# Optimization experiments

Hardware: AMD Instinct MI355X
Metric: run time of the kernel (lower is better)

## Reference

```python
import jax, jax.numpy as jnp
import numpy as np

B, S, HID = 2, 2048, 2560
NH, NKV, HD = 8, 4, 256
Q_SIZE, KV_SIZE = NH * HD, NKV * HD
SCALE = 256.0 ** -0.5
SLIDING_WINDOW = 1024 - 1  # config.sliding_window - 1
ROPE_BASE = 10000.0
EPS = 1e-6


def rmsnorm(x, w, eps=EPS):
    xf = x.astype(jnp.float32)
    out = xf * jax.lax.rsqrt(jnp.mean(xf * xf, axis=-1, keepdims=True) + eps)
    return (out * (1.0 + w.astype(jnp.float32))).astype(x.dtype)


def apply_rope(x, positions):
    # x: [B,S,H,D], neox style (rotate halves)
    d = x.shape[-1]
    inv_freq = 1.0 / (ROPE_BASE ** (jnp.arange(0, d, 2, dtype=jnp.float32) / d))
    freqs = positions.astype(jnp.float32)[..., None] * inv_freq  # [B,S,d/2]
    cos = jnp.cos(freqs)[:, :, None, :]
    sin = jnp.sin(freqs)[:, :, None, :]
    x1, x2 = x[..., : d // 2], x[..., d // 2:]
    return jnp.concatenate([x1 * cos - x2 * sin, x2 * cos + x1 * sin], axis=-1).astype(x.dtype)


def setup_inputs() -> dict:
    key = jax.random.key(0)
    ks = jax.random.split(key, 4)
    positions = jnp.broadcast_to(jnp.arange(S, dtype=jnp.int32)[None, :], (B, S))
    hidden_states = jax.random.normal(ks[0], (B, S, HID), dtype=jnp.float32)
    attention_mask = jnp.ones((B, S), dtype=jnp.int32)
    Wqkv = jax.random.normal(ks[1], (HID, Q_SIZE + 2 * KV_SIZE), dtype=jnp.float32) * (HID ** -0.5)
    Wo = jax.random.normal(ks[2], (Q_SIZE, HID), dtype=jnp.float32) * (Q_SIZE ** -0.5)
    q_norm_w = jnp.zeros((HD,), dtype=jnp.float32)
    k_norm_w = jnp.zeros((HD,), dtype=jnp.float32)
    return {"positions": positions, "hidden_states": hidden_states,
            "attention_mask": attention_mask, "Wqkv": Wqkv, "Wo": Wo,
            "q_norm_w": q_norm_w, "k_norm_w": k_norm_w}


def reference(positions, hidden_states, attention_mask, Wqkv, Wo, q_norm_w, k_norm_w):
    b, s, _ = hidden_states.shape
    qkv = hidden_states @ Wqkv
    q, k, v = jnp.split(qkv, [Q_SIZE, Q_SIZE + KV_SIZE], axis=-1)
    q = q.reshape(b, s, NH, HD)
    k = k.reshape(b, s, NKV, HD)
    v = v.reshape(b, s, NKV, HD)
    q = rmsnorm(q, q_norm_w)
    k = rmsnorm(k, k_norm_w)
    q = apply_rope(q, positions)
    k = apply_rope(k, positions)

    # additive mask, replicating source exactly
    idx = jnp.arange(s)
    causal = idx[None, :] > idx[:, None]             # triu(diag=1)
    too_far = (idx[None, :] - idx[:, None]) > SLIDING_WINDOW
    base_mask = causal | too_far                      # [S,S]
    key_pad = attention_mask.astype(bool) == False    # [B,S]
    masked = base_mask[None, None, :, :] | key_pad[:, None, None, :]  # [B,1,S,S]
    add_mask = jnp.where(masked, -jnp.inf, 0.0).astype(jnp.float32)

    # GQA: group queries over kv heads
    g = NH // NKV
    qg = q.reshape(b, s, NKV, g, HD)
    scores = jnp.einsum('bsmgd,btmd->bmgst', qg, k) * SCALE  # [B,NKV,g,S,S]
    scores = scores + add_mask[:, :, None, :, :]
    probs = jax.nn.softmax(scores, axis=-1)
    out = jnp.einsum('bmgst,btmd->bsmgd', probs, v)           # [B,S,NKV,g,HD]
    out = out.reshape(b, s, NH * HD)
    return out @ Wo
```

## Files before the change

kernel.cpp:

```cpp
#include <hip/hip_runtime.h>
#include <stdint.h>

#define S_LEN 2048
#define BATCH 2
#define HIDDEN 2560
#define NH 8
#define NKV 4
#define HD 256
#define QSZ (NH*HD)
#define NQKV 4096
#define MROWS (BATCH*S_LEN)
#define SCALE_ATT 0.0625f

using bf16x8 = __attribute__((__ext_vector_type__(8))) __bf16;
using f32x4  = __attribute__((__ext_vector_type__(4))) float;
using s16x8  = __attribute__((__ext_vector_type__(8))) short;

union B8u { s16x8 s; bf16x8 b; };
union I4B8 { int4 i; bf16x8 b; };

__device__ __forceinline__ unsigned short f2bf(float x){
  unsigned u = __float_as_uint(x);
  u += 0x7fffu + ((u >> 16) & 1u);
  return (unsigned short)(u >> 16);
}
__device__ __forceinline__ float bf2f(unsigned short h){
  return __uint_as_float(((unsigned)h) << 16);
}
__device__ __forceinline__ bf16x8 ld_bf8(const unsigned short* p){
  B8u u; u.s = *reinterpret_cast<const s16x8*>(p); return u.b;
}
__device__ __forceinline__ f32x4 mfma16(bf16x8 a, bf16x8 b, f32x4 c){
  return __builtin_amdgcn_mfma_f32_16x16x32_bf16(a, b, c, 0, 0, 0);
}
__device__ __forceinline__ void gload16(const void* g, void* l){
  __builtin_amdgcn_global_load_lds((const __attribute__((address_space(1))) void*)g,
                                   (__attribute__((address_space(3))) void*)l,
                                   16, 0, 0);
}
__device__ __forceinline__ int cvtpk(float lo, float hi){
  int r;
  asm("v_cvt_pk_bf16_f32 %0, %1, %2" : "=v"(r) : "v"(lo), "v"(hi));
  return r;
}

__global__ __launch_bounds__(256) void cast_bf16_kernel(
    const float* __restrict__ in, unsigned short* __restrict__ out, int n)
{
  int i = (blockIdx.x * 256 + threadIdx.x) * 4;
  if (i < n){
    float4 v = *reinterpret_cast<const float4*>(in + i);
    ushort4 o;
    o.x = f2bf(v.x); o.y = f2bf(v.y); o.z = f2bf(v.z); o.w = f2bf(v.w);
    *reinterpret_cast<ushort4*>(out + i) = o;
  }
}

__global__ __launch_bounds__(256) void tcast_kernel(
    const float* __restrict__ in, unsigned short* __restrict__ out, int R, int C)
{
  __shared__ float t[32][33];
  int c0 = blockIdx.x * 32, r0 = blockIdx.y * 32;
  int tx = threadIdx.x & 31, ty = threadIdx.x >> 5;
#pragma unroll
  for (int ii = 0; ii < 4; ii++)
    t[ty + ii*8][tx] = in[(size_t)(r0 + ty + ii*8) * C + c0 + tx];
  __syncthreads();
#pragma unroll
  for (int ii = 0; ii < 4; ii++)
    out[(size_t)(c0 + ty + ii*8) * R + r0 + tx] = f2bf(t[tx][ty + ii*8]);
}

template<int BF16OUT>
__global__ __launch_bounds__(512, 2) void gemm256_kernel(
    const unsigned short* __restrict__ A,
    const unsigned short* __restrict__ BT,
    void* __restrict__ Cv,
    int N, int K, int nbn)
{
  __shared__ unsigned short Ab[2][256 * 64];
  __shared__ unsigned short Bb[2][256 * 64];

  const int tid  = threadIdx.x;
  const int lane = tid & 63;
  const int wid  = tid >> 6;
  const int wm = wid >> 2, wn = wid & 3;
  const int lq = lane & 15, lk = lane >> 4;

  const int cpx = gridDim.x >> 3;
  const int wg  = (blockIdx.x & 7) * cpx + (blockIdx.x >> 3);
  const int bm = wg / nbn, bn = wg % nbn;

  const int l8 = lane >> 3;
  const int sl = ((lane & 7) ^ l8) * 8;
  const unsigned short* agS = A  + (size_t)(bm*256 + wid*16 + l8) * K + sl;
  const unsigned short* bgS = BT + (size_t)(bn*256 + wid*16 + l8) * K + sl;

  f32x4 acc[4][4][2] = {};
  bf16x8 a[4][2], b[2][2];

#define STA(c, h, tt) do {                                                    \
    unsigned short* d = &Ab[c][(h)*8192 + wid*1024];                          \
    const unsigned short* s = agS + (size_t)(h)*128*K + (size_t)(tt)*64;      \
    gload16(s, d); gload16(s + 8*(size_t)K, d + 512);                         \
  } while (0)
#define STB(c, h, tt) do {                                                    \
    unsigned short* d = &Bb[c][(h)*8192 + wid*1024];                          \
    const unsigned short* s = bgS + (size_t)(h)*128*K + (size_t)(tt)*64;      \
    gload16(s, d); gload16(s + 8*(size_t)K, d + 512);                         \
  } while (0)
#define LDA(qa) do {                                                          \
    _Pragma("unroll") for (int m = 0; m < 4; m++)                             \
    _Pragma("unroll") for (int kk = 0; kk < 2; kk++)                          \
      a[m][kk] = ld_bf8(&Ab[cur][((qa)*128 + wm*64 + m*16 + lq)*64            \
                                 + (((kk*4 + lk) ^ (lq & 7)) << 3)]);         \
  } while (0)
#define LDB(qb) do {                                                          \
    _Pragma("unroll") for (int n = 0; n < 2; n++)                             \
    _Pragma("unroll") for (int kk = 0; kk < 2; kk++)                          \
      b[n][kk] = ld_bf8(&Bb[cur][((qb)*128 + wn*32 + n*16 + lq)*64            \
                                 + (((kk*4 + lk) ^ (lq & 7)) << 3)]);         \
  } while (0)
#define MM(qi) do {                                                           \
    __builtin_amdgcn_s_setprio(1);                                            \
    _Pragma("unroll") for (int m = 0; m < 4; m++)                             \
    _Pragma("unroll") for (int n = 0; n < 2; n++)                             \
    _Pragma("unroll") for (int kk = 0; kk < 2; kk++)                          \
      acc[qi][m][n] = mfma16(a[m][kk], b[n][kk], acc[qi][m][n]);              \
    __builtin_amdgcn_s_setprio(0);                                            \
  } while (0)
#define BARR __builtin_amdgcn_s_barrier()
#define VM(n) asm volatile("s_waitcnt vmcnt(" #n ")" ::: "memory")

  STA(0, 0, 0); STB(0, 0, 0); STB(0, 1, 0); STA(0, 1, 0);
  VM(4); BARR;

  const int NT = K >> 6;
  for (int t = 0; t < NT - 1; ++t){
    const int cur = t & 1, nxt = cur ^ 1;
    LDA(0); LDB(0); STA(nxt, 0, t+1);
    BARR; MM(0); VM(4); BARR;
    LDB(1);         STB(nxt, 0, t+1);
    BARR; MM(1); VM(4); BARR;
    LDA(1);         STB(nxt, 1, t+1);
    BARR; MM(2);        BARR;
    LDB(0);         STA(nxt, 1, t+1);
    BARR; MM(3); VM(4); BARR;
  }
  {
    const int cur = (NT - 1) & 1;
    LDA(0); LDB(0); BARR; MM(0); VM(2); BARR;
    LDB(1);         BARR; MM(1); VM(0); BARR;
    LDA(1);         BARR; MM(2);        BARR;
    LDB(0);         BARR; MM(3);        BARR;
  }
#undef STA
#undef STB
#undef LDA
#undef LDB
#undef MM
#undef BARR
#undef VM

#pragma unroll
  for (int qi = 0; qi < 4; qi++){
    const int qa = qi >> 1;
    const int qb = (qi ^ (qi >> 1)) & 1;
    const int r0 = bm*256 + qa*128 + wm*64;
    const int c0 = bn*256 + qb*128 + wn*32;
#pragma unroll
    for (int m = 0; m < 4; m++)
#pragma unroll
      for (int n = 0; n < 2; n++)
#pragma unroll
        for (int i = 0; i < 4; i++){
          const size_t idx = (size_t)(r0 + m*16 + lk*4 + i) * N + (c0 + n*16 + lq);
          if (BF16OUT) ((unsigned short*)Cv)[idx] = f2bf(acc[qi][m][n][i]);
          else         ((float*)Cv)[idx]          = acc[qi][m][n][i];
        }
  }
}

__global__ __launch_bounds__(256) void normrope_kernel(
    const unsigned short* __restrict__ qkv,
    const int* __restrict__ positions,
    const float* __restrict__ qw, const float* __restrict__ kw,
    unsigned short* __restrict__ qB,
    unsigned short* __restrict__ kB,
    unsigned short* __restrict__ vT)
{
  const int s = blockIdx.x, b = blockIdx.y;
  const int lane = threadIdx.x & 63, wid = threadIdx.x >> 6;
  const unsigned short* row = qkv + (size_t)(b * S_LEN + s) * NQKV;
  const float fpos = (float)positions[b * S_LEN + s];

#pragma unroll
  for (int t = 0; t < 4; t++){
    const int seg = t * 4 + wid;
    const int base = seg * HD;
    float x0 = bf2f(row[base + lane]);
    float x1 = bf2f(row[base + lane + 64]);
    float x2 = bf2f(row[base + lane + 128]);
    float x3 = bf2f(row[base + lane + 192]);
    if (seg >= 12){
      const int mh = seg - 12;
      unsigned short* vb = vT + (size_t)(b * NKV + mh) * HD * S_LEN + s;
      vb[(size_t)(lane      ) * S_LEN] = f2bf(x0);
      vb[(size_t)(lane +  64) * S_LEN] = f2bf(x1);
      vb[(size_t)(lane + 128) * S_LEN] = f2bf(x2);
      vb[(size_t)(lane + 192) * S_LEN] = f2bf(x3);
    } else {
      const float* w = (seg < 8) ? qw : kw;
      float ssq = x0*x0 + x1*x1 + x2*x2 + x3*x3;
#pragma unroll
      for (int d = 1; d < 64; d <<= 1) ssq += __shfl_xor(ssq, d, 64);
      float rs = rsqrtf(ssq * (1.0f / 256.0f) + 1e-6f);
      float y0 = x0 * rs * (1.0f + w[lane]);
      float y1 = x1 * rs * (1.0f + w[lane + 64]);
      float y2 = x2 * rs * (1.0f + w[lane + 128]);
      float y3 = x3 * rs * (1.0f + w[lane + 192]);
      const float kln = -9.210340371976184f / 128.0f;
      float inv1 = expf((float)lane * kln);
      float inv2 = expf((float)(lane + 64) * kln);
      float s1, c1, s2, c2;
      sincosf(fpos * inv1, &s1, &c1);
      sincosf(fpos * inv2, &s2, &c2);
      float o0 = y0 * c1 - y2 * s1;
      float o2 = y2 * c1 + y0 * s1;
      float o1 = y1 * c2 - y3 * s2;
      float o3 = y3 * c2 + y1 * s2;
      unsigned short* dst = (seg < 8)
        ? qB + ((size_t)(b * NH  +  seg     ) * S_LEN + s) * HD
        : kB + ((size_t)(b * NKV + (seg - 8)) * S_LEN + s) * HD;
      dst[lane      ] = f2bf(o0);
      dst[lane +  64] = f2bf(o1);
      dst[lane + 128] = f2bf(o2);
      dst[lane + 192] = f2bf(o3);
    }
  }
}

__global__ void maskbits_kernel(const int* __restrict__ amask, unsigned* __restrict__ bm,
                                int* __restrict__ ctr)
{
  int t = threadIdx.x;
  int b = t >> 6, tile = t & 63;
  unsigned m = 0;
  for (int j = 0; j < 32; j++)
    m |= (amask[b * S_LEN + tile * 32 + j] != 0 ? 1u : 0u) << j;
  bm[t] = m;
  if (t < 8) ctr[t] = 0;
}

__global__ __launch_bounds__(256) void attn_kernel(
    const unsigned short* __restrict__ qB,
    const unsigned short* __restrict__ kB,
    const unsigned short* __restrict__ vT,
    const unsigned* __restrict__ bmG,
    unsigned short* __restrict__ attnO,
    int* __restrict__ ctr)
{
  __shared__ unsigned short Kb[2][32 * 256];
  __shared__ unsigned short Vb[2][256 * 32];
  __shared__ unsigned bm_lds[64];
  __shared__ int s_idx;

  const int tid  = threadIdx.x;
  const int lane = tid & 63, wid = tid >> 6;
  const int c  = blockIdx.x & 7;
  const int mh = c & 3, b = c >> 2;
  const int h  = mh * 2 + (wid >> 1);
  const int lq = lane & 15, lk = lane >> 4;

  if (tid < 64) bm_lds[tid] = bmG[(b << 6) + tid];

  const unsigned short* kbase = kB + (size_t)(b * NKV + mh) * S_LEN * HD;
  const unsigned short* vbase = vT + (size_t)(b * NKV + mh) * HD * S_LEN;
  const int krow0 = wid * 2 + (lane >> 5);
  const int kgsrc = (lane & 31) ^ (krow0 & 7);
  const unsigned short* kg0 = kbase + (size_t)krow0 * HD + kgsrc * 8;
  const int vd0 = wid * 16 + (lane >> 2);
  const int vgsrc = (lane & 3) ^ ((lane >> 3) & 3);
  const unsigned short* vg0 = vbase + (size_t)vd0 * S_LEN + vgsrc * 8;

#define STAGE_K(buf, ktv)                                                      \
  do {                                                                         \
    _Pragma("unroll")                                                          \
    for (int r = 0; r < 4; r++)                                                \
      gload16(kg0 + (size_t)(ktv) * HD + r * (8 * HD),                         \
              &Kb[buf][wid * 512 + r * 2048]);                                 \
  } while (0)
#define STAGE_V(buf, ktv)                                                      \
  do {                                                                         \
    _Pragma("unroll")                                                          \
    for (int r = 0; r < 4; r++)                                                \
      gload16(vg0 + (ktv) + (size_t)r * (64 * S_LEN),                          \
              &Vb[buf][wid * 512 + r * 2048]);                                 \
  } while (0)

  for (;;){
    if (tid == 0) s_idx = atomicAdd(&ctr[c], 1);
    __syncthreads();
    const int idx = s_idx;
    __syncthreads();
    if (idx >= 64) break;
    const int qt = 63 - idx;

    const int q0 = qt * 32 + (wid & 1) * 16;
    const int q  = q0 + lq;

    const unsigned short* qbase = qB + ((size_t)(b * NH + h) * S_LEN + q0 + lq) * HD + lk * 8;
    bf16x8 aq[8];
#pragma unroll
    for (int ks = 0; ks < 8; ks++) aq[ks] = ld_bf8(qbase + ks * 32);
    asm volatile("s_waitcnt vmcnt(0)" ::: "memory");

    float mi = -__builtin_inff(), li = 0.f;
    f32x4 oacc[16] = {};

    const int ktmax = qt * 32;

    STAGE_K(0, 0);  STAGE_V(0, 0);
    if (ktmax >= 32){ STAGE_K(1, 32); STAGE_V(1, 32); }

    int cur = 0;
    for (int kt = 0; kt <= ktmax; kt += 32, cur ^= 1){
      if (kt < ktmax) asm volatile("s_waitcnt vmcnt(8)" ::: "memory");
      else            asm volatile("s_waitcnt vmcnt(0)" ::: "memory");
      __syncthreads();

      f32x4 s0 = {0.f,0.f,0.f,0.f}, s1 = {0.f,0.f,0.f,0.f};
#pragma unroll
      for (int ks = 0; ks < 8; ks++){
        const int slot = (((ks * 4 + lk) ^ (lq & 7)) << 3);
        bf16x8 kf0 = ld_bf8(&Kb[cur][lq * 256 + slot]);
        bf16x8 kf1 = ld_bf8(&Kb[cur][(16 + lq) * 256 + slot]);
        s0 = mfma16(kf0, aq[ks], s0);
        s1 = mfma16(kf1, aq[ks], s1);
      }

      const unsigned mask32 = bm_lds[kt >> 5];
      const int koff = lk * 4;
      float v0[4], v1[4];
#pragma unroll
      for (int j2 = 0; j2 < 4; j2++){
        const bool cc0 = (kt + koff + j2 <= q)      && ((mask32 >> (koff + j2)) & 1u);
        const bool cc1 = (kt + 16 + koff + j2 <= q) && ((mask32 >> (16 + koff + j2)) & 1u);
        v0[j2] = cc0 ? s0[j2] * SCALE_ATT : -__builtin_inff();
        v1[j2] = cc1 ? s1[j2] * SCALE_ATT : -__builtin_inff();
      }
      float tm = fmaxf(fmaxf(fmaxf(v0[0], v0[1]), fmaxf(v0[2], v0[3])),
                       fmaxf(fmaxf(v1[0], v1[1]), fmaxf(v1[2], v1[3])));
      tm = fmaxf(tm, __shfl_xor(tm, 16, 64));
      tm = fmaxf(tm, __shfl_xor(tm, 32, 64));

      float p0[4], p1[4];
      if (__all(tm <= mi + 8.0f)){
        const float mns = fmaxf(mi, -1e30f);
#pragma unroll
        for (int j2 = 0; j2 < 4; j2++){
          p0[j2] = __expf(v0[j2] - mns);
          p1[j2] = __expf(v1[j2] - mns);
        }
        float rs = (p0[0] + p0[1]) + (p0[2] + p0[3]) + (p1[0] + p1[1]) + (p1[2] + p1[3]);
        rs += __shfl_xor(rs, 16, 64);
        rs += __shfl_xor(rs, 32, 64);
        li += rs;
      } else {
        const float mn  = fmaxf(mi, tm);
        const float mns = fmaxf(mn, -1e30f);
#pragma unroll
        for (int j2 = 0; j2 < 4; j2++){
          p0[j2] = __expf(v0[j2] - mns);
          p1[j2] = __expf(v1[j2] - mns);
        }
        const float a_ = __expf(mi - mns);
        float rs = (p0[0] + p0[1]) + (p0[2] + p0[3]) + (p1[0] + p1[1]) + (p1[2] + p1[3]);
        rs += __shfl_xor(rs, 16, 64);
        rs += __shfl_xor(rs, 32, 64);
        li = li * a_ + rs;
        mi = mn;
        float av[4];
#pragma unroll
        for (int i = 0; i < 4; i++)
          av[i] = __shfl(a_, (lane & 48) | (lk * 4 + i), 64);
#pragma unroll
        for (int db = 0; db < 16; db++){
          f32x4 o = oacc[db];
#pragma unroll
          for (int i = 0; i < 4; i++) o[i] *= av[i];
          oacc[db] = o;
        }
      }

      const int w0 = cvtpk(p0[0], p0[1]), w1 = cvtpk(p0[2], p0[3]);
      const int w2 = cvtpk(p1[0], p1[1]), w3 = cvtpk(p1[2], p1[3]);
      const int sA = (((lk & 1) * 2) << 4) | lq;
      const int sB = sA + 16;
      const int a0 = __shfl(w0, sA, 64), a1 = __shfl(w1, sA, 64);
      const int b0 = __shfl(w0, sB, 64), b1 = __shfl(w1, sB, 64);
      const int c0w = __shfl(w2, sA, 64), c1w = __shfl(w3, sA, 64);
      const int d0w = __shfl(w2, sB, 64), d1w = __shfl(w3, sB, 64);
      const bool hi = (lk >= 2);
      I4B8 pau;
      pau.i.x = hi ? c0w : a0;
      pau.i.y = hi ? c1w : a1;
      pau.i.z = hi ? d0w : b0;
      pau.i.w = hi ? d1w : b1;

      const int vslot = (lk ^ ((lq >> 1) & 3)) << 3;
#pragma unroll
      for (int db = 0; db < 16; db++){
        bf16x8 vf = ld_bf8(&Vb[cur][(db * 16 + lq) * 32 + vslot]);
        oacc[db] = mfma16(pau.b, vf, oacc[db]);
      }

      __syncthreads();
      if (kt + 64 <= ktmax){ STAGE_K(cur, kt + 64); STAGE_V(cur, kt + 64); }
    }

#pragma unroll
    for (int i = 0; i < 4; i++){
      const float lf = __shfl(li, (lane & 48) | (lk * 4 + i), 64);
      const float inv = 1.0f / lf;
      unsigned short* orow = attnO + (size_t)(b * S_LEN + q0 + lk*4 + i) * QSZ + h * HD + lq;
#pragma unroll
      for (int db = 0; db < 16; db++)
        orow[db * 16] = f2bf(oacc[db][i] * inv);
    }
  }
#undef STAGE_K
#undef STAGE_V
}

extern "C" void kernel_launch(void* const* d_in, const int* in_sizes, int n_in,
                              void* d_out, int out_size, void* d_ws, size_t ws_size,
                              hipStream_t stream)
{
  const int*   positions = (const int*)  d_in[0];
  const float* hidden    = (const float*)d_in[1];
  const int*   amask     = (const int*)  d_in[2];
  const float* Wqkv      = (const float*)d_in[3];
  const float* Wo        = (const float*)d_in[4];
  const float* qw        = (const float*)d_in[5];
  const float* kw        = (const float*)d_in[6];
  float* out = (float*)d_out;

  char* ws = (char*)d_ws;
  unsigned short* hB    = (unsigned short*)(ws);
  unsigned short* attnO = (unsigned short*)(ws);
  unsigned short* WqT   = (unsigned short*)(ws + 20971520);
  unsigned short* WoT   = (unsigned short*)(ws + 41943040);
  unsigned short* qkvB  = (unsigned short*)(ws + 52428800);
  unsigned short* qb    = (unsigned short*)(ws + 119537664);
  unsigned short* kb    = (unsigned short*)(ws + 136314880);
  unsigned short* vt    = (unsigned short*)(ws + 144703488);
  unsigned*       bm    = (unsigned*)     (ws + 153092096);
  int*            ctr   = (int*)          (ws + 153092608);

  cast_bf16_kernel<<<dim3(MROWS * HIDDEN / 1024), 256, 0, stream>>>(hidden, hB, MROWS * HIDDEN);
  tcast_kernel<<<dim3(NQKV / 32, HIDDEN / 32), 256, 0, stream>>>(Wqkv, WqT, HIDDEN, NQKV);
  tcast_kernel<<<dim3(HIDDEN / 32, QSZ / 32), 256, 0, stream>>>(Wo, WoT, QSZ, HIDDEN);
  maskbits_kernel<<<dim3(1), 128, 0, stream>>>(amask, bm, ctr);

  gemm256_kernel<1><<<dim3((MROWS/256) * (NQKV/256)), 512, 0, stream>>>(
      hB, WqT, qkvB, NQKV, HIDDEN, NQKV/256);

  normrope_kernel<<<dim3(S_LEN, BATCH), 256, 0, stream>>>(qkvB, positions, qw, kw, qb, kb, vt);

  attn_kernel<<<dim3(256), 256, 0, stream>>>(qb, kb, vt, bm, attnO, ctr);

  gemm256_kernel<0><<<dim3((MROWS/256) * (HIDDEN/256)), 512, 0, stream>>>(
      attnO, WoT, out, HIDDEN, QSZ, HIDDEN/256);
}
```

Before: 338.5 us.

## Split attention key range across wave pairs with LDS merge of partial softmax

Each work item now covers a 16-row query tile instead of 32, and the two waves per head split the key tiles into even and odd 32-key blocks, keeping separate online-softmax state. After the loop, one wave writes its partial output and max/sum to shared memory, and the other merges both with rescaling before writing bf16 output. K and V staging is split so K for the next step is prefetched during the softmax phase and V after the PV product. The grid doubles to 512 blocks to give finer-grained work units. The cost is extra barriers per iteration and an LDS merge pass at the end.

```diff
diff --git a/kernel.cpp b/kernel.cpp
--- a/kernel.cpp
+++ b/kernel.cpp
@@ -260,16 +260,18 @@
     unsigned short* __restrict__ attnO,
     int* __restrict__ ctr)
 {
-  __shared__ unsigned short Kb[2][32 * 256];
-  __shared__ unsigned short Vb[2][256 * 32];
+  __shared__ unsigned short Ks[2][32 * 256];
+  __shared__ unsigned short Vs[2][256 * 32];
   __shared__ unsigned bm_lds[64];
+  __shared__ float mlbuf[2][2][16];
   __shared__ int s_idx;
 
   const int tid  = threadIdx.x;
   const int lane = tid & 63, wid = tid >> 6;
   const int c  = blockIdx.x & 7;
   const int mh = c & 3, b = c >> 2;
-  const int h  = mh * 2 + (wid >> 1);
+  const int hh = wid >> 1, sp = wid & 1;
+  const int h  = mh * 2 + hh;
   const int lq = lane & 15, lk = lane >> 4;
 
   if (tid < 64) bm_lds[tid] = bmG[(b << 6) + tid];
@@ -283,19 +285,33 @@
   const int vgsrc = (lane & 3) ^ ((lane >> 3) & 3);
   const unsigned short* vg0 = vbase + (size_t)vd0 * S_LEN + vgsrc * 8;
 
-#define STAGE_K(buf, ktv)                                                      \
+  float* obuf = (float*)&Ks[0][0];
+
+#define STAGE_K2(it1)                                                          \
   do {                                                                         \
+    const int ka = min((it1) * 64,      S_LEN - 32);                           \
+    const int kb2 = min((it1) * 64 + 32, S_LEN - 32);                          \
     _Pragma("unroll")                                                          \
     for (int r = 0; r < 4; r++)                                                \
-      gload16(kg0 + (size_t)(ktv) * HD + r * (8 * HD),                         \
-              &Kb[buf][wid * 512 + r * 2048]);                                 \
-  } while (0)
-#define STAGE_V(buf, ktv)                                                      \
-  do {                                                                         \
+      gload16(kg0 + (size_t)ka * HD + r * (8 * HD),                            \
+              &Ks[0][wid * 512 + r * 2048]);                                   \
     _Pragma("unroll")                                                          \
     for (int r = 0; r < 4; r++)                                                \
-      gload16(vg0 + (ktv) + (size_t)r * (64 * S_LEN),                          \
-              &Vb[buf][wid * 512 + r * 2048]);                                 \
+      gload16(kg0 + (size_t)kb2 * HD + r * (8 * HD),                           \
+              &Ks[1][wid * 512 + r * 2048]);                                   \
+  } while (0)
+#define STAGE_V2(it1)                                                          \
+  do {                                                                         \
+    const int ka = min((it1) * 64,      S_LEN - 32);                           \
+    const int kb2 = min((it1) * 64 + 32, S_LEN - 32);                          \
+    _Pragma("unroll")                                                          \
+    for (int r = 0; r < 4; r++)                                                \
+      gload16(vg0 + ka  + (size_t)r * (64 * S_LEN),                            \
+              &Vs[0][wid * 512 + r * 2048]);                                   \
+    _Pragma("unroll")                                                          \
+    for (int r = 0; r < 4; r++)                                                \
+      gload16(vg0 + kb2 + (size_t)r * (64 * S_LEN),                            \
+              &Vs[1][wid * 512 + r * 2048]);                                   \
   } while (0)
 
   for (;;){
@@ -303,11 +319,12 @@
     __syncthreads();
     const int idx = s_idx;
     __syncthreads();
-    if (idx >= 64) break;
-    const int qt = 63 - idx;
-
-    const int q0 = qt * 32 + (wid & 1) * 16;
+    if (idx >= 128) break;
+    const int qt16 = 127 - idx;
+    const int q0 = qt16 * 16;
     const int q  = q0 + lq;
+    const int nt = (qt16 >> 1) + 1;
+    const int L  = (nt + 1) >> 1;
 
     const unsigned short* qbase = qB + ((size_t)(b * NH + h) * S_LEN + q0 + lq) * HD + lk * 8;
     bf16x8 aq[8];
@@ -318,28 +335,30 @@
     float mi = -__builtin_inff(), li = 0.f;
     f32x4 oacc[16] = {};
 
-    const int ktmax = qt * 32;
-
-    STAGE_K(0, 0);  STAGE_V(0, 0);
-    if (ktmax >= 32){ STAGE_K(1, 32); STAGE_V(1, 32); }
-
-    int cur = 0;
-    for (int kt = 0; kt <= ktmax; kt += 32, cur ^= 1){
-      if (kt < ktmax) asm volatile("s_waitcnt vmcnt(8)" ::: "memory");
-      else            asm volatile("s_waitcnt vmcnt(0)" ::: "memory");
+    STAGE_K2(0);
+    STAGE_V2(0);
+
+    for (int it = 0; it < L; ++it){
+      const bool more = (it + 1 < L);
+      const int kt = it * 64 + sp * 32;
+
+      asm volatile("s_waitcnt vmcnt(8)" ::: "memory");
       __syncthreads();
 
       f32x4 s0 = {0.f,0.f,0.f,0.f}, s1 = {0.f,0.f,0.f,0.f};
 #pragma unroll
       for (int ks = 0; ks < 8; ks++){
         const int slot = (((ks * 4 + lk) ^ (lq & 7)) << 3);
-        bf16x8 kf0 = ld_bf8(&Kb[cur][lq * 256 + slot]);
-        bf16x8 kf1 = ld_bf8(&Kb[cur][(16 + lq) * 256 + slot]);
+        bf16x8 kf0 = ld_bf8(&Ks[sp][lq * 256 + slot]);
+        bf16x8 kf1 = ld_bf8(&Ks[sp][(16 + lq) * 256 + slot]);
         s0 = mfma16(kf0, aq[ks], s0);
         s1 = mfma16(kf1, aq[ks], s1);
       }
 
-      const unsigned mask32 = bm_lds[kt >> 5];
+      __syncthreads();
+      if (more) STAGE_K2(it + 1);
+
+      const unsigned mask32 = bm_lds[(kt >> 5) & 63];
       const int koff = lk * 4;
       float v0[4], v1[4];
 #pragma unroll
@@ -408,29 +427,63 @@
       pau.i.z = hi ? d0w : b0;
       pau.i.w = hi ? d1w : b1;
 
+      if (more) asm volatile("s_waitcnt vmcnt(8)" ::: "memory");
+      else      asm volatile("s_waitcnt vmcnt(0)" ::: "memory");
+      __syncthreads();
+
       const int vslot = (lk ^ ((lq >> 1) & 3)) << 3;
 #pragma unroll
       for (int db = 0; db < 16; db++){
-        bf16x8 vf = ld_bf8(&Vb[cur][(db * 16 + lq) * 32 + vslot]);
+        bf16x8 vf = ld_bf8(&Vs[sp][(db * 16 + lq) * 32 + vslot]);
         oacc[db] = mfma16(pau.b, vf, oacc[db]);
       }
 
       __syncthreads();
-      if (kt + 64 <= ktmax){ STAGE_K(cur, kt + 64); STAGE_V(cur, kt + 64); }
+      if (more) STAGE_V2(it + 1);
     }
 
-#pragma unroll
-    for (int i = 0; i < 4; i++){
-      const float lf = __shfl(li, (lane & 48) | (lk * 4 + i), 64);
-      const float inv = 1.0f / lf;
-      unsigned short* orow = attnO + (size_t)(b * S_LEN + q0 + lk*4 + i) * QSZ + h * HD + lq;
+    if (sp){
+      if (lk == 0){
+        mlbuf[hh][0][lq] = mi;
+        mlbuf[hh][1][lq] = li;
+      }
 #pragma unroll
       for (int db = 0; db < 16; db++)
-        orow[db * 16] = f2bf(oacc[db][i] * inv);
+#pragma unroll
+        for (int i = 0; i < 4; i++)
+          obuf[hh * 4096 + (lk*4 + i) * 256 + db*16 + lq] = oacc[db][i];
     }
+    __syncthreads();
+    if (!sp){
+      const float m1 = mlbuf[hh][0][lq];
+      const float l1 = mlbuf[hh][1][lq];
+      const float ms  = fmaxf(mi, m1);
+      const float msf = fmaxf(ms, -1e30f);
+      const float a0f = __expf(mi - msf);
+      const float a1f = __expf(m1 - msf);
+      const float inv = 1.0f / (li * a0f + l1 * a1f);
+      const float s0f = a0f * inv, s1f = a1f * inv;
+      float sc0[4], sc1[4];
+#pragma unroll
+      for (int i = 0; i < 4; i++){
+        sc0[i] = __shfl(s0f, (lane & 48) | (lk*4 + i), 64);
+        sc1[i] = __shfl(s1f, (lane & 48) | (lk*4 + i), 64);
+      }
+#pragma unroll
+      for (int i = 0; i < 4; i++){
+        unsigned short* orow = attnO + (size_t)(b * S_LEN + q0 + lk*4 + i) * QSZ + h * HD + lq;
+#pragma unroll
+        for (int db = 0; db < 16; db++){
+          float v = oacc[db][i] * sc0[i]
+                  + obuf[hh * 4096 + (lk*4 + i) * 256 + db*16 + lq] * sc1[i];
+          orow[db * 16] = f2bf(v);
+        }
+      }
+    }
+    __syncthreads();
   }
-#undef STAGE_K
-#undef STAGE_V
+#undef STAGE_K2
+#undef STAGE_V2
 }
 
 extern "C" void kernel_launch(void* const* d_in, const int* in_sizes, int n_in,
@@ -468,7 +521,7 @@
 
   normrope_kernel<<<dim3(S_LEN, BATCH), 256, 0, stream>>>(qkvB, positions, qw, kw, qb, kb, vt);
 
-  attn_kernel<<<dim3(256), 256, 0, stream>>>(qb, kb, vt, bm, attnO, ctr);
+  attn_kernel<<<dim3(512), 256, 0, stream>>>(qb, kb, vt, bm, attnO, ctr);
 
   gemm256_kernel<0><<<dim3((MROWS/256) * (HIDDEN/256)), 512, 0, stream>>>(
       attnO, WoT, out, HIDDEN, QSZ, HIDDEN/256);
```

Measured after the change: 362.3 us. 7.0% more time.

## Process key tiles in pairs with four-deep K/V LDS pipeline

Applied to the files above, without the earlier changes.

The attention loop now handles two 32-key tiles per iteration, computing both score blocks before one shared online-softmax update, with one max/sum reduction and one rescale per pair. K/V staging grows from double to quadruple buffering, so more global loads are in flight and barriers per key tile are halved. The cost is double the LDS footprint (about 128KB), which may cut occupancy, plus extra registers for the second score block and branches for an odd final tile.

```diff
diff --git a/kernel.cpp b/kernel.cpp
--- a/kernel.cpp
+++ b/kernel.cpp
@@ -260,8 +260,8 @@
     unsigned short* __restrict__ attnO,
     int* __restrict__ ctr)
 {
-  __shared__ unsigned short Kb[2][32 * 256];
-  __shared__ unsigned short Vb[2][256 * 32];
+  __shared__ unsigned short Kb[4][32 * 256];
+  __shared__ unsigned short Vb[4][256 * 32];
   __shared__ unsigned bm_lds[64];
   __shared__ int s_idx;
 
@@ -318,51 +318,93 @@
     float mi = -__builtin_inff(), li = 0.f;
     f32x4 oacc[16] = {};
 
-    const int ktmax = qt * 32;
-
-    STAGE_K(0, 0);  STAGE_V(0, 0);
-    if (ktmax >= 32){ STAGE_K(1, 32); STAGE_V(1, 32); }
-
-    int cur = 0;
-    for (int kt = 0; kt <= ktmax; kt += 32, cur ^= 1){
-      if (kt < ktmax) asm volatile("s_waitcnt vmcnt(8)" ::: "memory");
-      else            asm volatile("s_waitcnt vmcnt(0)" ::: "memory");
+    STAGE_K(0, 0); STAGE_V(0, 0);
+    if (qt >= 1){ STAGE_K(1, 32); STAGE_V(1, 32); }
+    if (qt >= 2){ STAGE_K(2, 64); STAGE_V(2, 64); }
+    if (qt >= 3){ STAGE_K(3, 96); STAGE_V(3, 96); }
+
+    const int npairs = (qt >> 1) + 1;
+    for (int p = 0; p < npairs; ++p){
+      const int ktA = p * 64;
+      const int ktB = ktA + 32;
+      const bool hasB = (2*p + 1 <= qt);
+      const int bufA = (2*p) & 3, bufB = (2*p + 1) & 3;
+
+      const int ahead = qt - 2*p - 1;
+      if (ahead >= 2)      asm volatile("s_waitcnt vmcnt(16)" ::: "memory");
+      else if (ahead == 1) asm volatile("s_waitcnt vmcnt(8)"  ::: "memory");
+      else                 asm volatile("s_waitcnt vmcnt(0)"  ::: "memory");
       __syncthreads();
 
-      f32x4 s0 = {0.f,0.f,0.f,0.f}, s1 = {0.f,0.f,0.f,0.f};
-#pragma unroll
-      for (int ks = 0; ks < 8; ks++){
-        const int slot = (((ks * 4 + lk) ^ (lq & 7)) << 3);
-        bf16x8 kf0 = ld_bf8(&Kb[cur][lq * 256 + slot]);
-        bf16x8 kf1 = ld_bf8(&Kb[cur][(16 + lq) * 256 + slot]);
-        s0 = mfma16(kf0, aq[ks], s0);
-        s1 = mfma16(kf1, aq[ks], s1);
-      }
-
-      const unsigned mask32 = bm_lds[kt >> 5];
+      f32x4 sA0 = {0.f,0.f,0.f,0.f}, sA1 = {0.f,0.f,0.f,0.f};
+      f32x4 sB0 = {0.f,0.f,0.f,0.f}, sB1 = {0.f,0.f,0.f,0.f};
+      if (hasB){
+#pragma unroll
+        for (int ks = 0; ks < 8; ks++){
+          const int slot = (((ks * 4 + lk) ^ (lq & 7)) << 3);
+          bf16x8 kA0 = ld_bf8(&Kb[bufA][lq * 256 + slot]);
+          bf16x8 kA1 = ld_bf8(&Kb[bufA][(16 + lq) * 256 + slot]);
+          bf16x8 kB0 = ld_bf8(&Kb[bufB][lq * 256 + slot]);
+          bf16x8 kB1 = ld_bf8(&Kb[bufB][(16 + lq) * 256 + slot]);
+          sA0 = mfma16(kA0, aq[ks], sA0);
+          sA1 = mfma16(kA1, aq[ks], sA1);
+          sB0 = mfma16(kB0, aq[ks], sB0);
+          sB1 = mfma16(kB1, aq[ks], sB1);
+        }
+      } else {
+#pragma unroll
+        for (int ks = 0; ks < 8; ks++){
+          const int slot = (((ks * 4 + lk) ^ (lq & 7)) << 3);
+          bf16x8 kA0 = ld_bf8(&Kb[bufA][lq * 256 + slot]);
+          bf16x8 kA1 = ld_bf8(&Kb[bufA][(16 + lq) * 256 + slot]);
+          sA0 = mfma16(kA0, aq[ks], sA0);
+          sA1 = mfma16(kA1, aq[ks], sA1);
+        }
+      }
+
+      const unsigned mA = bm_lds[ktA >> 5];
+      const unsigned mB = bm_lds[(ktB >> 5) & 63];
       const int koff = lk * 4;
-      float v0[4], v1[4];
+      float vA0[4], vA1[4], vB0[4], vB1[4];
 #pragma unroll
       for (int j2 = 0; j2 < 4; j2++){
-        const bool cc0 = (kt + koff + j2 <= q)      && ((mask32 >> (koff + j2)) & 1u);
-        const bool cc1 = (kt + 16 + koff + j2 <= q) && ((mask32 >> (16 + koff + j2)) & 1u);
-        v0[j2] = cc0 ? s0[j2] * SCALE_ATT : -__builtin_inff();
-        v1[j2] = cc1 ? s1[j2] * SCALE_ATT : -__builtin_inff();
-      }
-      float tm = fmaxf(fmaxf(fmaxf(v0[0], v0[1]), fmaxf(v0[2], v0[3])),
-                       fmaxf(fmaxf(v1[0], v1[1]), fmaxf(v1[2], v1[3])));
+        const bool a0 = (ktA + koff + j2 <= q)      && ((mA >> (koff + j2)) & 1u);
+        const bool a1 = (ktA + 16 + koff + j2 <= q) && ((mA >> (16 + koff + j2)) & 1u);
+        vA0[j2] = a0 ? sA0[j2] * SCALE_ATT : -__builtin_inff();
+        vA1[j2] = a1 ? sA1[j2] * SCALE_ATT : -__builtin_inff();
+      }
+      if (hasB){
+#pragma unroll
+        for (int j2 = 0; j2 < 4; j2++){
+          const bool b0 = (ktB + koff + j2 <= q)      && ((mB >> (koff + j2)) & 1u);
+          const bool b1 = (ktB + 16 + koff + j2 <= q) && ((mB >> (16 + koff + j2)) & 1u);
+          vB0[j2] = b0 ? sB0[j2] * SCALE_ATT : -__builtin_inff();
+          vB1[j2] = b1 ? sB1[j2] * SCALE_ATT : -__builtin_inff();
+        }
+      } else {
+#pragma unroll
+        for (int j2 = 0; j2 < 4; j2++){ vB0[j2] = -__builtin_inff(); vB1[j2] = -__builtin_inff(); }
+      }
+      float tm = fmaxf(fmaxf(fmaxf(vA0[0], vA0[1]), fmaxf(vA0[2], vA0[3])),
+                       fmaxf(fmaxf(vA1[0], vA1[1]), fmaxf(vA1[2], vA1[3])));
+      if (hasB){
+        float tb = fmaxf(fmaxf(fmaxf(vB0[0], vB0[1]), fmaxf(vB0[2], vB0[3])),
+                         fmaxf(fmaxf(vB1[0], vB1[1]), fmaxf(vB1[2], vB1[3])));
+        tm = fmaxf(tm, tb);
+      }
       tm = fmaxf(tm, __shfl_xor(tm, 16, 64));
       tm = fmaxf(tm, __shfl_xor(tm, 32, 64));
 
-      float p0[4], p1[4];
+      float pA0[4], pA1[4], pB0[4], pB1[4];
       if (__all(tm <= mi + 8.0f)){
         const float mns = fmaxf(mi, -1e30f);
 #pragma unroll
         for (int j2 = 0; j2 < 4; j2++){
-          p0[j2] = __expf(v0[j2] - mns);
-          p1[j2] = __expf(v1[j2] - mns);
-        }
-        float rs = (p0[0] + p0[1]) + (p0[2] + p0[3]) + (p1[0] + p1[1]) + (p1[2] + p1[3]);
+          pA0[j2] = __expf(vA0[j2] - mns); pA1[j2] = __expf(vA1[j2] - mns);
+          pB0[j2] = __expf(vB0[j2] - mns); pB1[j2] = __expf(vB1[j2] - mns);
+        }
+        float rs = (pA0[0]+pA0[1])+(pA0[2]+pA0[3])+(pA1[0]+pA1[1])+(pA1[2]+pA1[3])
+                 + (pB0[0]+pB0[1])+(pB0[2]+pB0[3])+(pB1[0]+pB1[1])+(pB1[2]+pB1[3]);
         rs += __shfl_xor(rs, 16, 64);
         rs += __shfl_xor(rs, 32, 64);
         li += rs;
@@ -371,11 +413,12 @@
         const float mns = fmaxf(mn, -1e30f);
 #pragma unroll
         for (int j2 = 0; j2 < 4; j2++){
-          p0[j2] = __expf(v0[j2] - mns);
-          p1[j2] = __expf(v1[j2] - mns);
+          pA0[j2] = __expf(vA0[j2] - mns); pA1[j2] = __expf(vA1[j2] - mns);
+          pB0[j2] = __expf(vB0[j2] - mns); pB1[j2] = __expf(vB1[j2] - mns);
         }
         const float a_ = __expf(mi - mns);
-        float rs = (p0[0] + p0[1]) + (p0[2] + p0[3]) + (p1[0] + p1[1]) + (p1[2] + p1[3]);
+        float rs = (pA0[0]+pA0[1])+(pA0[2]+pA0[3])+(pA1[0]+pA1[1])+(pA1[2]+pA1[3])
+                 + (pB0[0]+pB0[1])+(pB0[2]+pB0[3])+(pB1[0]+pB1[1])+(pB1[2]+pB1[3]);
         rs += __shfl_xor(rs, 16, 64);
         rs += __shfl_xor(rs, 32, 64);
         li = li * a_ + rs;
@@ -393,30 +436,55 @@
         }
       }
 
-      const int w0 = cvtpk(p0[0], p0[1]), w1 = cvtpk(p0[2], p0[3]);
-      const int w2 = cvtpk(p1[0], p1[1]), w3 = cvtpk(p1[2], p1[3]);
-      const int sA = (((lk & 1) * 2) << 4) | lq;
-      const int sB = sA + 16;
-      const int a0 = __shfl(w0, sA, 64), a1 = __shfl(w1, sA, 64);
-      const int b0 = __shfl(w0, sB, 64), b1 = __shfl(w1, sB, 64);
-      const int c0w = __shfl(w2, sA, 64), c1w = __shfl(w3, sA, 64);
-      const int d0w = __shfl(w2, sB, 64), d1w = __shfl(w3, sB, 64);
+      const int sA_ = (((lk & 1) * 2) << 4) | lq;
+      const int sB_ = sA_ + 16;
       const bool hi = (lk >= 2);
-      I4B8 pau;
-      pau.i.x = hi ? c0w : a0;
-      pau.i.y = hi ? c1w : a1;
-      pau.i.z = hi ? d0w : b0;
-      pau.i.w = hi ? d1w : b1;
+      I4B8 pauA, pauB;
+      {
+        const int w0 = cvtpk(pA0[0], pA0[1]), w1 = cvtpk(pA0[2], pA0[3]);
+        const int w2 = cvtpk(pA1[0], pA1[1]), w3 = cvtpk(pA1[2], pA1[3]);
+        const int a0 = __shfl(w0, sA_, 64), a1 = __shfl(w1, sA_, 64);
+        const int b0 = __shfl(w0, sB_, 64), b1 = __shfl(w1, sB_, 64);
+        const int c0w = __shfl(w2, sA_, 64), c1w = __shfl(w3, sA_, 64);
+        const int d0w = __shfl(w2, sB_, 64), d1w = __shfl(w3, sB_, 64);
+        pauA.i.x = hi ? c0w : a0;
+        pauA.i.y = hi ? c1w : a1;
+        pauA.i.z = hi ? d0w : b0;
+        pauA.i.w = hi ? d1w : b1;
+      }
+      if (hasB){
+        const int w0 = cvtpk(pB0[0], pB0[1]), w1 = cvtpk(pB0[2], pB0[3]);
+        const int w2 = cvtpk(pB1[0], pB1[1]), w3 = cvtpk(pB1[2], pB1[3]);
+        const int a0 = __shfl(w0, sA_, 64), a1 = __shfl(w1, sA_, 64);
+        const int b0 = __shfl(w0, sB_, 64), b1 = __shfl(w1, sB_, 64);
+        const int c0w = __shfl(w2, sA_, 64), c1w = __shfl(w3, sA_, 64);
+        const int d0w = __shfl(w2, sB_, 64), d1w = __shfl(w3, sB_, 64);
+        pauB.i.x = hi ? c0w : a0;
+        pauB.i.y = hi ? c1w : a1;
+        pauB.i.z = hi ? d0w : b0;
+        pauB.i.w = hi ? d1w : b1;
+      }
 
       const int vslot = (lk ^ ((lq >> 1) & 3)) << 3;
-#pragma unroll
-      for (int db = 0; db < 16; db++){
-        bf16x8 vf = ld_bf8(&Vb[cur][(db * 16 + lq) * 32 + vslot]);
-        oacc[db] = mfma16(pau.b, vf, oacc[db]);
+      if (hasB){
+#pragma unroll
+        for (int db = 0; db < 16; db++){
+          bf16x8 vfA = ld_bf8(&Vb[bufA][(db * 16 + lq) * 32 + vslot]);
+          bf16x8 vfB = ld_bf8(&Vb[bufB][(db * 16 + lq) * 32 + vslot]);
+          f32x4 o = mfma16(pauA.b, vfA, oacc[db]);
+          oacc[db] = mfma16(pauB.b, vfB, o);
+        }
+      } else {
+#pragma unroll
+        for (int db = 0; db < 16; db++){
+          bf16x8 vfA = ld_bf8(&Vb[bufA][(db * 16 + lq) * 32 + vslot]);
+          oacc[db] = mfma16(pauA.b, vfA, oacc[db]);
+        }
       }
 
       __syncthreads();
-      if (kt + 64 <= ktmax){ STAGE_K(cur, kt + 64); STAGE_V(cur, kt + 64); }
+      if (2*p + 4 <= qt){ STAGE_K(bufA, ktA + 128); STAGE_V(bufA, ktA + 128); }
+      if (2*p + 5 <= qt){ STAGE_K(bufB, ktB + 128); STAGE_V(bufB, ktB + 128); }
     }
 
 #pragma unroll
```

New measurement: 336.4 us. Within noise of the previous version (-0.6%).
